# Kernel tuning notes

Measured on AMD Instinct MI355X. Metric: run time of the kernel, lower is better.

Reference implementation:

```python
import jax, jax.numpy as jnp
import numpy as np

REG_WEIGHT = 1.0
VAR_WEIGHT = 0.01

# Flattened skeleton pairs (group-major) from VarLoss
_ID1 = np.array([0, 1, 3, 4, 10, 11, 13, 14, 2, 3, 12, 13])
_ID2 = np.array([1, 2, 4, 5, 11, 12, 14, 15, 6, 6, 8, 8])
_WGT = np.array([1.0085885098415446, 1.0, 1.0, 1.0085885098415446,
                 1.1375361376887123, 1.0, 1.0, 1.1375361376887123,
                 1.0, 1.0, 1.0, 1.0], dtype=np.float32)
_GID = np.array([0, 0, 0, 0, 1, 1, 1, 1, 2, 2, 3, 3])
_G = np.eye(4, dtype=np.float32)[_GID]  # [12, 4] one-hot group membership


def setup_inputs() -> dict:
    key = jax.random.key(0)
    k1, k2, k3, k4, k5 = jax.random.split(key, 5)
    B, K, H, W = 256, 16, 256, 256
    output = jax.random.normal(k1, (B, 1, H, W), dtype=jnp.float32)
    mask = jax.random.randint(k2, (B, K), 0, 2, dtype=jnp.int32)
    # make half the batch fully unmasked so the VarLoss branch (mask.sum()==0) fires
    mask = mask.at[: B // 2].set(0)
    ind = jax.random.randint(k3, (B, K), 0, H * W, dtype=jnp.int32)
    target = jax.random.uniform(k4, (B, K, 1), dtype=jnp.float32)  # also 'visible' via >0.5
    gt_2d = jax.random.normal(k5, (B, 2 * K), dtype=jnp.float32)
    return {"output": output, "mask": mask, "ind": ind, "target": target, "gt_2d": gt_2d}


def _fusion_loss(output, mask, ind, target, gt_2d):
    B = output.shape[0]
    # _tranpose_and_gather_scalar: [B,1,H,W] -> [B,HW,1], gather K indices
    feat = output.transpose(0, 2, 3, 1).reshape(B, -1, 1)
    pred = jnp.take_along_axis(feat, ind[:, :, None].astype(jnp.int32), axis=1)  # [B,K,1]

    # reg_loss: masked smooth-L1 (sum) / num_visible
    m = mask.astype(pred.dtype)
    num = m.sum()
    d = (pred - target) * m[:, :, None]
    ad = jnp.abs(d)
    sl1 = jnp.where(ad < 1.0, 0.5 * ad * ad, ad - 0.5).sum()
    reg = sl1 / (num + 0.0001)

    # VarLoss: per-group variance of weighted 3D bone lengths, only for samples with mask.sum()==0
    xy = gt_2d.reshape(B, -1, 2)               # [B,K,2]
    z = pred[:, :, 0]                          # [B,K]
    dxy2 = ((xy[:, _ID1] - xy[:, _ID2]) ** 2).sum(-1)   # [B,12]
    dz = z[:, _ID1] - z[:, _ID2]
    l = jnp.sqrt(dxy2 + dz * dz) * jnp.asarray(_WGT)     # weighted lengths [B,12]
    vis = (target[:, _ID1, 0] > 0.5) & (target[:, _ID2, 0] > 0.5)
    visf = vis.astype(l.dtype)
    G = jnp.asarray(_G)
    num_g = visf @ G                           # [B,4] visible pairs per group
    sum_g = (l * visf) @ G                     # [B,4]
    E = jnp.where(num_g > 0.5, sum_g / jnp.maximum(num_g, 1.0), 0.0)
    Ep = E[:, _GID]                            # [B,12] group mean per pair
    ng = jnp.maximum(num_g[:, _GID], 1.0)
    term = jnp.where(vis & (l > 0), (l - Ep) ** 2 / (2.0 * ng), 0.0)
    per_sample = term.sum(1)                   # [B]
    sample_ok = (mask.sum(1) == 0)
    var = jnp.where(sample_ok, per_sample, 0.0).sum() / B

    return REG_WEIGHT * reg + VAR_WEIGHT * var


def reference(output, mask, ind, target, gt_2d):
    return _fusion_loss(output, mask, ind, target, gt_2d)
```

## Files before the change

### kernel.cpp

```cpp
#include <hip/hip_runtime.h>


#define B_   256
#define K_   16
#define HW_  65536

__global__ __launch_bounds__(256, 1)
void FusionLoss_kernel(const float* __restrict__ output,
                       const int*   __restrict__ mask,
                       const int*   __restrict__ ind,
                       const float* __restrict__ target,
                       const float* __restrict__ gt2d,
                       float*       __restrict__ out) {
    const int b = threadIdx.x;

    float pred[K_], tgt[K_];
    float sl1 = 0.0f;
    float num = 0.0f;
    int   msum = 0;
    #pragma unroll
    for (int k = 0; k < K_; ++k) {
        const int idx = ind[b * K_ + k];
        const float p = output[b * HW_ + idx];
        const float t = target[b * K_ + k];
        pred[k] = p;
        tgt[k]  = t;
        const int mk = mask[b * K_ + k];
        msum += mk;
        if (mk) {
            const float ad = fabsf(p - t);
            sl1 += (ad < 1.0f) ? 0.5f * ad * ad : (ad - 0.5f);
            num += 1.0f;
        }
    }

    float x[K_], y[K_];
    #pragma unroll
    for (int j = 0; j < K_; ++j) {
        x[j] = gt2d[b * 2 * K_ + 2 * j];
        y[j] = gt2d[b * 2 * K_ + 2 * j + 1];
    }

    const int   id1[12] = {0, 1, 3, 4, 10, 11, 13, 14, 2, 3, 12, 13};
    const int   id2[12] = {1, 2, 4, 5, 11, 12, 14, 15, 6, 6,  8,  8};
    const float wgt[12] = {1.0085885098415446f, 1.0f, 1.0f, 1.0085885098415446f,
                           1.1375361376887123f, 1.0f, 1.0f, 1.1375361376887123f,
                           1.0f, 1.0f, 1.0f, 1.0f};
    const int   gid[12] = {0, 0, 0, 0, 1, 1, 1, 1, 2, 2, 3, 3};

    float l[12];
    bool  vis[12];
    float num_g[4] = {0.f, 0.f, 0.f, 0.f};
    float sum_g[4] = {0.f, 0.f, 0.f, 0.f};
    #pragma unroll
    for (int e = 0; e < 12; ++e) {
        const int i1 = id1[e], i2 = id2[e];
        const float dx = x[i1] - x[i2];
        const float dy = y[i1] - y[i2];
        const float dz = pred[i1] - pred[i2];
        const float le = sqrtf(dx * dx + dy * dy + dz * dz) * wgt[e];
        l[e] = le;
        const bool v = (tgt[i1] > 0.5f) && (tgt[i2] > 0.5f);
        vis[e] = v;
        if (v) {
            num_g[gid[e]] += 1.0f;
            sum_g[gid[e]] += le;
        }
    }

    float E[4], ng4[4];
    #pragma unroll
    for (int g = 0; g < 4; ++g) {
        const float n = num_g[g];
        ng4[g] = fmaxf(n, 1.0f);
        E[g]   = (n > 0.5f) ? (sum_g[g] / ng4[g]) : 0.0f;
    }

    float per = 0.0f;
    #pragma unroll
    for (int e = 0; e < 12; ++e) {
        if (vis[e] && (l[e] > 0.0f)) {
            const float d = l[e] - E[gid[e]];
            per += d * d / (2.0f * ng4[gid[e]]);
        }
    }
    float var_c = (msum == 0) ? per : 0.0f;

    #pragma unroll
    for (int off = 32; off > 0; off >>= 1) {
        sl1   += __shfl_down(sl1,   off);
        num   += __shfl_down(num,   off);
        var_c += __shfl_down(var_c, off);
    }
    __shared__ float s_sl1[4], s_num[4], s_var[4];
    const int wave = threadIdx.x >> 6;
    const int lane = threadIdx.x & 63;
    if (lane == 0) {
        s_sl1[wave] = sl1;
        s_num[wave] = num;
        s_var[wave] = var_c;
    }
    __syncthreads();
    if (threadIdx.x == 0) {
        float tsl1 = 0.f, tnum = 0.f, tvar = 0.f;
        #pragma unroll
        for (int w = 0; w < 4; ++w) {
            tsl1 += s_sl1[w];
            tnum += s_num[w];
            tvar += s_var[w];
        }
        const float reg = tsl1 / (tnum + 0.0001f);
        const float var = tvar / (float)B_;
        out[0] = 1.0f * reg + 0.01f * var;
    }
}

extern "C" void kernel_launch(void* const* d_in, const int* in_sizes, int n_in,
                              void* d_out, int out_size, void* d_ws, size_t ws_size,
                              hipStream_t stream) {
    const float* output = (const float*)d_in[0];
    const int*   mask   = (const int*)  d_in[1];
    const int*   ind    = (const int*)  d_in[2];
    const float* target = (const float*)d_in[3];
    const float* gt2d   = (const float*)d_in[4];
    float* out = (float*)d_out;

    FusionLoss_kernel<<<1, 256, 0, stream>>>(output, mask, ind, target, gt2d, out);
}
```

Baseline: 107.2 us.

## Split fusion loss into per-sample blocks plus a separate final reduction kernel

The single-block kernel, where each of 256 threads handled one sample serially, becomes two kernels. The first launches one 64-thread block per sample; 16 lanes gather the predictions in parallel into shared memory, lane 0 computes the bone-length variance term, and the block writes a float4 partial to workspace. A second single-block kernel reduces the 256 partials into the scalar loss. This spreads the latency-bound scattered gathers across many CUs, at the cost of an extra kernel launch and a workspace round trip.

Measured after the change: 95.82 us (median of 2 runs). -10.6%, faster.

```diff
diff --git a/kernel.cpp b/kernel.cpp
--- a/kernel.cpp
+++ b/kernel.cpp
@@ -5,103 +5,121 @@
 #define K_   16
 #define HW_  65536
 
-__global__ __launch_bounds__(256, 1)
-void FusionLoss_kernel(const float* __restrict__ output,
-                       const int*   __restrict__ mask,
-                       const int*   __restrict__ ind,
-                       const float* __restrict__ target,
-                       const float* __restrict__ gt2d,
-                       float*       __restrict__ out) {
-    const int b = threadIdx.x;
+__global__ __launch_bounds__(64, 8)
+void fusion_partial(const float* __restrict__ output,
+                    const int*   __restrict__ mask,
+                    const int*   __restrict__ ind,
+                    const float* __restrict__ target,
+                    const float* __restrict__ gt2d,
+                    float4*      __restrict__ partial) {
+    const int b    = blockIdx.x;
+    const int lane = threadIdx.x;
 
-    float pred[K_], tgt[K_];
-    float sl1 = 0.0f;
-    float num = 0.0f;
-    int   msum = 0;
-    #pragma unroll
-    for (int k = 0; k < K_; ++k) {
-        const int idx = ind[b * K_ + k];
-        const float p = output[b * HW_ + idx];
-        const float t = target[b * K_ + k];
-        pred[k] = p;
-        tgt[k]  = t;
-        const int mk = mask[b * K_ + k];
-        msum += mk;
+    __shared__ float s_pred[K_];
+    __shared__ float s_tgt[K_];
+    __shared__ float s_xy[2 * K_];
+
+    float psl1 = 0.0f, pnum = 0.0f;
+    int   pm   = 0;
+
+    if (lane < 2 * K_) s_xy[lane] = gt2d[b * 2 * K_ + lane];
+    if (lane < K_) {
+        const int   idx = ind[b * K_ + lane];
+        const float p   = output[b * HW_ + idx];
+        const float t   = target[b * K_ + lane];
+        const int   mk  = mask[b * K_ + lane];
+        s_pred[lane] = p;
+        s_tgt[lane]  = t;
+        pm = mk;
         if (mk) {
             const float ad = fabsf(p - t);
-            sl1 += (ad < 1.0f) ? 0.5f * ad * ad : (ad - 0.5f);
-            num += 1.0f;
+            psl1 = (ad < 1.0f) ? 0.5f * ad * ad : (ad - 0.5f);
+            pnum = 1.0f;
         }
     }
 
-    float x[K_], y[K_];
     #pragma unroll
-    for (int j = 0; j < K_; ++j) {
-        x[j] = gt2d[b * 2 * K_ + 2 * j];
-        y[j] = gt2d[b * 2 * K_ + 2 * j + 1];
+    for (int off = 8; off > 0; off >>= 1) {
+        psl1 += __shfl_down(psl1, off);
+        pnum += __shfl_down(pnum, off);
+        pm   += __shfl_down(pm,   off);
     }
 
-    const int   id1[12] = {0, 1, 3, 4, 10, 11, 13, 14, 2, 3, 12, 13};
-    const int   id2[12] = {1, 2, 4, 5, 11, 12, 14, 15, 6, 6,  8,  8};
-    const float wgt[12] = {1.0085885098415446f, 1.0f, 1.0f, 1.0085885098415446f,
-                           1.1375361376887123f, 1.0f, 1.0f, 1.1375361376887123f,
-                           1.0f, 1.0f, 1.0f, 1.0f};
-    const int   gid[12] = {0, 0, 0, 0, 1, 1, 1, 1, 2, 2, 3, 3};
+    __syncthreads();
 
-    float l[12];
-    bool  vis[12];
-    float num_g[4] = {0.f, 0.f, 0.f, 0.f};
-    float sum_g[4] = {0.f, 0.f, 0.f, 0.f};
-    #pragma unroll
-    for (int e = 0; e < 12; ++e) {
-        const int i1 = id1[e], i2 = id2[e];
-        const float dx = x[i1] - x[i2];
-        const float dy = y[i1] - y[i2];
-        const float dz = pred[i1] - pred[i2];
-        const float le = sqrtf(dx * dx + dy * dy + dz * dz) * wgt[e];
-        l[e] = le;
-        const bool v = (tgt[i1] > 0.5f) && (tgt[i2] > 0.5f);
-        vis[e] = v;
-        if (v) {
-            num_g[gid[e]] += 1.0f;
-            sum_g[gid[e]] += le;
+    if (lane == 0) {
+        const int   id1[12] = {0, 1, 3, 4, 10, 11, 13, 14, 2, 3, 12, 13};
+        const int   id2[12] = {1, 2, 4, 5, 11, 12, 14, 15, 6, 6,  8,  8};
+        const float wgt[12] = {1.0085885098415446f, 1.0f, 1.0f, 1.0085885098415446f,
+                               1.1375361376887123f, 1.0f, 1.0f, 1.1375361376887123f,
+                               1.0f, 1.0f, 1.0f, 1.0f};
+        const int   gid[12] = {0, 0, 0, 0, 1, 1, 1, 1, 2, 2, 3, 3};
+
+        float l[12];
+        bool  vis[12];
+        float num_g[4] = {0.f, 0.f, 0.f, 0.f};
+        float sum_g[4] = {0.f, 0.f, 0.f, 0.f};
+        #pragma unroll
+        for (int e = 0; e < 12; ++e) {
+            const int i1 = id1[e], i2 = id2[e];
+            const float dx = s_xy[2 * i1]     - s_xy[2 * i2];
+            const float dy = s_xy[2 * i1 + 1] - s_xy[2 * i2 + 1];
+            const float dz = s_pred[i1] - s_pred[i2];
+            const float le = sqrtf(dx * dx + dy * dy + dz * dz) * wgt[e];
+            l[e] = le;
+            const bool v = (s_tgt[i1] > 0.5f) && (s_tgt[i2] > 0.5f);
+            vis[e] = v;
+            if (v) {
+                num_g[gid[e]] += 1.0f;
+                sum_g[gid[e]] += le;
+            }
         }
+
+        float E[4], ng4[4];
+        #pragma unroll
+        for (int g = 0; g < 4; ++g) {
+            const float n = num_g[g];
+            ng4[g] = fmaxf(n, 1.0f);
+            E[g]   = (n > 0.5f) ? (sum_g[g] / ng4[g]) : 0.0f;
+        }
+
+        float per = 0.0f;
+        #pragma unroll
+        for (int e = 0; e < 12; ++e) {
+            if (vis[e] && (l[e] > 0.0f)) {
+                const float d = l[e] - E[gid[e]];
+                per += d * d / (2.0f * ng4[gid[e]]);
+            }
+        }
+        const float var_c = (pm == 0) ? per : 0.0f;
+
+        partial[b] = make_float4(psl1, pnum, var_c, 0.0f);
     }
+}
 
-    float E[4], ng4[4];
-    #pragma unroll
-    for (int g = 0; g < 4; ++g) {
-        const float n = num_g[g];
-        ng4[g] = fmaxf(n, 1.0f);
-        E[g]   = (n > 0.5f) ? (sum_g[g] / ng4[g]) : 0.0f;
-    }
-
-    float per = 0.0f;
-    #pragma unroll
-    for (int e = 0; e < 12; ++e) {
-        if (vis[e] && (l[e] > 0.0f)) {
-            const float d = l[e] - E[gid[e]];
-            per += d * d / (2.0f * ng4[gid[e]]);
-        }
-    }
-    float var_c = (msum == 0) ? per : 0.0f;
+__global__ __launch_bounds__(256, 1)
+void fusion_final(const float4* __restrict__ partial,
+                  float*        __restrict__ out) {
+    const int t = threadIdx.x;
+    const float4 v = partial[t];
+    float sl1 = v.x, num = v.y, var = v.z;
 
     #pragma unroll
     for (int off = 32; off > 0; off >>= 1) {
-        sl1   += __shfl_down(sl1,   off);
-        num   += __shfl_down(num,   off);
-        var_c += __shfl_down(var_c, off);
+        sl1 += __shfl_down(sl1, off);
+        num += __shfl_down(num, off);
+        var += __shfl_down(var, off);
     }
     __shared__ float s_sl1[4], s_num[4], s_var[4];
-    const int wave = threadIdx.x >> 6;
-    const int lane = threadIdx.x & 63;
+    const int wave = t >> 6;
+    const int lane = t & 63;
     if (lane == 0) {
         s_sl1[wave] = sl1;
         s_num[wave] = num;
-        s_var[wave] = var_c;
+        s_var[wave] = var;
     }
     __syncthreads();
-    if (threadIdx.x == 0) {
+    if (t == 0) {
         float tsl1 = 0.f, tnum = 0.f, tvar = 0.f;
         #pragma unroll
         for (int w = 0; w < 4; ++w) {
@@ -109,9 +127,7 @@
             tnum += s_num[w];
             tvar += s_var[w];
         }
-        const float reg = tsl1 / (tnum + 0.0001f);
-        const float var = tvar / (float)B_;
-        out[0] = 1.0f * reg + 0.01f * var;
+        out[0] = tsl1 / (tnum + 0.0001f) + 0.01f * (tvar / (float)B_);
     }
 }
 
@@ -123,7 +139,9 @@
     const int*   ind    = (const int*)  d_in[2];
     const float* target = (const float*)d_in[3];
     const float* gt2d   = (const float*)d_in[4];
-    float* out = (float*)d_out;
+    float*  out     = (float*)d_out;
+    float4* partial = (float4*)d_ws;
 
-    FusionLoss_kernel<<<1, 256, 0, stream>>>(output, mask, ind, target, gt2d, out);
+    fusion_partial<<<B_, 64, 0, stream>>>(output, mask, ind, target, gt2d, partial);
+    fusion_final<<<1, 256, 0, stream>>>(partial, out);
 }
```
